# Performance work log

Measured on AMD Instinct MI355X. Metric: run time of the kernel, lower is better.

Reference implementation:

```python
import jax, jax.numpy as jnp
import numpy as np

B, D, C, H = 64, 64, 128, 64  # batch, feature dim, channels, MLP hidden

def setup_inputs() -> dict:
    key = jax.random.key(0)
    k1, k2, k3, kp = jax.random.split(key, 4)
    x = jax.random.normal(k1, (B, D, C), dtype=jnp.float32)
    W1 = jax.random.normal(k2, (2 * D, H), dtype=jnp.float32) / np.sqrt(2.0 * D).astype(np.float32)
    b1 = jnp.zeros((H,), jnp.float32)
    W2 = jax.random.normal(k3, (H, 1), dtype=jnp.float32) / np.sqrt(float(H)).astype(np.float32)
    b2 = jnp.zeros((1,), jnp.float32)
    perm = jax.random.permutation(kp, B)  # replaces torch.randperm(B)
    return {"x": x, "W1": W1, "b1": b1, "W2": W2, "b2": b2, "perm": perm}

def reference(x, W1, b1, W2, b2, perm):
    xt = jnp.transpose(x, (0, 2, 1))          # [B, C, D]
    b, c, d = xt.shape
    iu, ju = jnp.triu_indices(c, k=1)         # P = C*(C-1)//2 pairs (static)
    xi = xt[:, iu, :]                         # [B, P, D]
    xj = xt[:, ju, :]                         # [B, P, D]

    def T(h):                                  # h: [B, P, 2D] -> [B, P]
        z = jax.nn.relu(jnp.einsum('bpd,dh->bph', h, W1) + b1)
        return jnp.einsum('bph,ho->bp', z, W2) + b2[0]

    joint_term = T(jnp.concatenate([xi, xj], axis=-1))            # [B, P]
    marginal_term = T(jnp.concatenate([xi, xj[perm]], axis=-1))   # [B, P]
    lse = jax.nn.logsumexp(marginal_term, axis=0)                 # [P]
    mi_per_pair = joint_term - lse + jnp.log(jnp.float32(b))      # [B, P]
    total_mi = mi_per_pair.sum(axis=1).mean()
    n_pairs = c * (c - 1) // 2
    return -total_mi / n_pairs
```

## Files before the change

### kernel.cpp

```cpp
#include <hip/hip_runtime.h>
#include <hip/hip_bf16.h>
#include <math.h>

#define CC 128
#define BB 64
#define DD 64
#define HH 64
#define NPAIRS 8128
#define CHUNK 4
#define NBLK2 (NPAIRS / CHUNK)

struct Slots { double j; double l; };

#define OFF(i) ((i)*127 - ((i)*((i)-1))/2)

__global__ __launch_bounds__(256) void k1_tables(
    const float* __restrict__ x, const float* __restrict__ W1,
    const float* __restrict__ b1,
    float* __restrict__ A1, float* __restrict__ B2)
{
    __shared__ float xs[64][32];
    __shared__ float w1s[128][64];
    int b  = blockIdx.x >> 2;
    int cq = blockIdx.x & 3;

    for (int idx = threadIdx.x; idx < 2048; idx += 256)
        ((float4*)w1s)[idx] = ((const float4*)W1)[idx];
    for (int idx = threadIdx.x; idx < 2048; idx += 256) {
        int d = idx >> 5, cl = idx & 31;
        xs[d][cl] = x[((size_t)b * 64 + d) * 128 + cq * 32 + cl];
    }
    __syncthreads();

    int h  = threadIdx.x & 63;
    int c0 = (threadIdx.x >> 6) * 8;

    float accA[8] = {0,0,0,0,0,0,0,0};
    float accB[8] = {0,0,0,0,0,0,0,0};
    for (int d = 0; d < 64; ++d) {
        float wa = w1s[d][h];
        float wb = w1s[64 + d][h];
        float xv[8];
        *(float4*)&xv[0] = *(const float4*)&xs[d][c0];
        *(float4*)&xv[4] = *(const float4*)&xs[d][c0 + 4];
        #pragma unroll
        for (int k = 0; k < 8; ++k) {
            accA[k] = fmaf(xv[k], wa, accA[k]);
            accB[k] = fmaf(xv[k], wb, accB[k]);
        }
    }
    float bias = b1[h];
    #pragma unroll
    for (int k = 0; k < 8; ++k) {
        int c = cq * 32 + c0 + k;
        size_t o = ((size_t)b * CC + c) * HH + h;
        A1[o] = accA[k] + bias;
        B2[o] = accB[k];
    }
}

__global__ __launch_bounds__(64) void k2_pairs(
    const float* __restrict__ A1, const float* __restrict__ B2,
    const int* __restrict__ perm, const float* __restrict__ W2,
    Slots* __restrict__ slots)
{
    int lane = threadIdx.x;
    __shared__ int invp_s[64];
    invp_s[perm[lane]] = lane;
    __syncthreads();
    int ip = invp_s[lane];

    const float4* __restrict__ W2v = (const float4*)W2;

    float4 a1r[16], a2r[16];
    float accJ[CHUNK], accM[CHUNK];

    int p0 = blockIdx.x * CHUNK;
    double tt = 127.5 - sqrt(127.5 * 127.5 - 2.0 * (double)p0);
    int i = (int)tt;
    if (i < 0) i = 0;
    if (i > 126) i = 126;
    while (i < 126 && OFF(i + 1) <= p0) ++i;
    while (i > 0 && OFF(i) > p0) --i;
    int j = i + 1 + (p0 - OFF(i));

    bool need_load = true;
    for (int k = 0; k < CHUNK; ++k) {
        if (need_load) {
            const float4* ar1 = (const float4*)(A1 + ((size_t)lane * CC + i) * HH);
            const float4* ar2 = (const float4*)(A1 + ((size_t)ip   * CC + i) * HH);
            #pragma unroll
            for (int q = 0; q < 16; ++q) { a1r[q] = ar1[q]; a2r[q] = ar2[q]; }
            need_load = false;
        }
        const float4* br = (const float4*)(B2 + ((size_t)lane * CC + j) * HH);
        float aJ = 0.f, aM = 0.f;
        #pragma unroll
        for (int q = 0; q < 16; ++q) {
            float4 bq = br[q];
            float4 w  = W2v[q];
            aJ = fmaf(fmaxf(a1r[q].x + bq.x, 0.f), w.x, aJ);
            aJ = fmaf(fmaxf(a1r[q].y + bq.y, 0.f), w.y, aJ);
            aJ = fmaf(fmaxf(a1r[q].z + bq.z, 0.f), w.z, aJ);
            aJ = fmaf(fmaxf(a1r[q].w + bq.w, 0.f), w.w, aJ);
            aM = fmaf(fmaxf(a2r[q].x + bq.x, 0.f), w.x, aM);
            aM = fmaf(fmaxf(a2r[q].y + bq.y, 0.f), w.y, aM);
            aM = fmaf(fmaxf(a2r[q].z + bq.z, 0.f), w.z, aM);
            aM = fmaf(fmaxf(a2r[q].w + bq.w, 0.f), w.w, aM);
        }
        accJ[k] = aJ; accM[k] = aM;
        ++j;
        if (j == CC) { ++i; j = i + 1; need_load = true; }
    }

    float m[CHUNK], e[CHUNK];
    #pragma unroll
    for (int k = 0; k < CHUNK; ++k) m[k] = accM[k];
    #pragma unroll
    for (int off = 32; off > 0; off >>= 1) {
        #pragma unroll
        for (int k = 0; k < CHUNK; ++k)
            m[k] = fmaxf(m[k], __shfl_xor(m[k], off));
    }
    #pragma unroll
    for (int k = 0; k < CHUNK; ++k) e[k] = __expf(accM[k] - m[k]);
    #pragma unroll
    for (int off = 32; off > 0; off >>= 1) {
        #pragma unroll
        for (int k = 0; k < CHUNK; ++k)
            e[k] += __shfl_xor(e[k], off);
    }
    float lsum = 0.f;
    #pragma unroll
    for (int k = 0; k < CHUNK; ++k) lsum += m[k] + __logf(e[k]);

    float js = 0.f;
    #pragma unroll
    for (int k = 0; k < CHUNK; ++k) js += accJ[k];
    #pragma unroll
    for (int off = 32; off > 0; off >>= 1)
        js += __shfl_xor(js, off);

    if (lane == 0) { slots[blockIdx.x].j = (double)js; slots[blockIdx.x].l = (double)lsum; }
}

__global__ __launch_bounds__(256) void k3_final(
    const Slots* __restrict__ slots, float* __restrict__ out)
{
    __shared__ double sj[4], sl[4];
    double jd = 0.0, ld = 0.0;
    for (int s = threadIdx.x; s < NBLK2; s += 256) {
        jd += slots[s].j;
        ld += slots[s].l;
    }
    #pragma unroll
    for (int off = 32; off > 0; off >>= 1) {
        jd += __shfl_xor(jd, off);
        ld += __shfl_xor(ld, off);
    }
    int w = threadIdx.x >> 6;
    if ((threadIdx.x & 63) == 0) { sj[w] = jd; sl[w] = ld; }
    __syncthreads();
    if (threadIdx.x == 0) {
        jd = sj[0] + sj[1] + sj[2] + sj[3];
        ld = sl[0] + sl[1] + sl[2] + sl[3];
        double total = jd / 64.0 - ld + 8128.0 * log(64.0);
        out[0] = (float)(-total / 8128.0);
    }
}

extern "C" void kernel_launch(void* const* d_in, const int* in_sizes, int n_in,
                              void* d_out, int out_size, void* d_ws, size_t ws_size,
                              hipStream_t stream)
{
    const float* x   = (const float*)d_in[0];
    const float* W1  = (const float*)d_in[1];
    const float* b1  = (const float*)d_in[2];
    const float* W2  = (const float*)d_in[3];
    const int*  perm = (const int*)d_in[5];

    char* ws = (char*)d_ws;
    Slots* slots = (Slots*)ws;
    float* A1 = (float*)(ws + 40960);
    float* B2 = A1 + (size_t)BB * CC * HH;

    k1_tables<<<256, 256, 0, stream>>>(x, W1, b1, A1, B2);
    k2_pairs<<<NBLK2, 64, 0, stream>>>(A1, B2, perm, W2, slots);
    k3_final<<<1, 256, 0, stream>>>(slots, (float*)d_out);
}
```

Baseline: 104.6 us.

## Tile channel pairs into 4x4 blocks with LDS-staged B2 slabs

The pair kernel now gives each 256-thread block a 4x4 tile of upper-triangular channel pairs, 528 tiles in all, with one wave per row channel i. The B2 rows for the four j channels are staged once in swizzled shared memory and reused by all four waves. Each wave's A1 rows stay in registers across the four j values. Previously every pair reloaded its B2 row from global memory per lane, so this cuts global traffic by roughly the tile factor. The cost is some wasted arithmetic on the diagonal tiles, which is masked out, plus an extra block-level reduction and LDS use.

```diff
diff --git a/kernel.cpp b/kernel.cpp
--- a/kernel.cpp
+++ b/kernel.cpp
@@ -6,13 +6,10 @@
 #define BB 64
 #define DD 64
 #define HH 64
-#define NPAIRS 8128
-#define CHUNK 4
-#define NBLK2 (NPAIRS / CHUNK)
+#define NTILE 32
+#define NBLK2 528
 
 struct Slots { double j; double l; };
-
-#define OFF(i) ((i)*127 - ((i)*((i)-1))/2)
 
 __global__ __launch_bounds__(256) void k1_tables(
     const float* __restrict__ x, const float* __restrict__ W1,
@@ -59,89 +56,111 @@
     }
 }
 
-__global__ __launch_bounds__(64) void k2_pairs(
+__global__ __launch_bounds__(256, 2) void k2_pairs(
     const float* __restrict__ A1, const float* __restrict__ B2,
     const int* __restrict__ perm, const float* __restrict__ W2,
     Slots* __restrict__ slots)
 {
-    int lane = threadIdx.x;
+    __shared__ float4 bslab[4][64][16];
     __shared__ int invp_s[64];
+    __shared__ float wj[4], wl[4];
+
+    int t    = threadIdx.x;
+    int lane = t & 63;
+    int w    = t >> 6;
+
     invp_s[perm[lane]] = lane;
-    __syncthreads();
     int ip = invp_s[lane];
 
+    int u = blockIdx.x;
+    int r = 0;
+    while (((r + 1) * NTILE - ((r + 1) * r) / 2) <= u) ++r;
+    int tj = r + (u - (r * NTILE - (r * (r - 1)) / 2));
+    int i0 = r * 4, j0 = tj * 4;
+    bool diag = (tj == r);
+    int i = i0 + w;
+
+    const float4* a1p = (const float4*)(A1 + (size_t)lane * 8192 + (size_t)i * 64);
+    const float4* a2p = (const float4*)(A1 + (size_t)ip   * 8192 + (size_t)i * 64);
+    float4 a1r[16], a2r[16];
+    #pragma unroll
+    for (int q = 0; q < 16; ++q) a1r[q] = a1p[q];
+    #pragma unroll
+    for (int q = 0; q < 16; ++q) a2r[q] = a2p[q];
+
+    #pragma unroll
+    for (int rr = 0; rr < 16; ++rr) {
+        int fidx = rr * 256 + t;
+        int s = fidx >> 10;
+        int b = (fidx >> 4) & 63;
+        int q = fidx & 15;
+        float4 v = *(const float4*)(B2 + (size_t)b * 8192 + (size_t)(j0 + s) * 64 + (size_t)q * 4);
+        bslab[s][b][q ^ (b & 15)] = v;
+    }
+    __syncthreads();
+
     const float4* __restrict__ W2v = (const float4*)W2;
 
-    float4 a1r[16], a2r[16];
-    float accJ[CHUNK], accM[CHUNK];
-
-    int p0 = blockIdx.x * CHUNK;
-    double tt = 127.5 - sqrt(127.5 * 127.5 - 2.0 * (double)p0);
-    int i = (int)tt;
-    if (i < 0) i = 0;
-    if (i > 126) i = 126;
-    while (i < 126 && OFF(i + 1) <= p0) ++i;
-    while (i > 0 && OFF(i) > p0) --i;
-    int j = i + 1 + (p0 - OFF(i));
-
-    bool need_load = true;
-    for (int k = 0; k < CHUNK; ++k) {
-        if (need_load) {
-            const float4* ar1 = (const float4*)(A1 + ((size_t)lane * CC + i) * HH);
-            const float4* ar2 = (const float4*)(A1 + ((size_t)ip   * CC + i) * HH);
-            #pragma unroll
-            for (int q = 0; q < 16; ++q) { a1r[q] = ar1[q]; a2r[q] = ar2[q]; }
-            need_load = false;
+    float accJ[4], accM[4];
+    #pragma unroll
+    for (int jl = 0; jl < 4; ++jl) {
+        float aJ = 0.f, aM = 0.f;
+        #pragma unroll
+        for (int q = 0; q < 16; ++q) {
+            float4 bq = bslab[jl][lane][q ^ (lane & 15)];
+            float4 wv = W2v[q];
+            aJ = fmaf(fmaxf(a1r[q].x + bq.x, 0.f), wv.x, aJ);
+            aJ = fmaf(fmaxf(a1r[q].y + bq.y, 0.f), wv.y, aJ);
+            aJ = fmaf(fmaxf(a1r[q].z + bq.z, 0.f), wv.z, aJ);
+            aJ = fmaf(fmaxf(a1r[q].w + bq.w, 0.f), wv.w, aJ);
+            aM = fmaf(fmaxf(a2r[q].x + bq.x, 0.f), wv.x, aM);
+            aM = fmaf(fmaxf(a2r[q].y + bq.y, 0.f), wv.y, aM);
+            aM = fmaf(fmaxf(a2r[q].z + bq.z, 0.f), wv.z, aM);
+            aM = fmaf(fmaxf(a2r[q].w + bq.w, 0.f), wv.w, aM);
         }
-        const float4* br = (const float4*)(B2 + ((size_t)lane * CC + j) * HH);
-        float aJ = 0.f, aM = 0.f;
-        #pragma unroll
-        for (int q = 0; q < 16; ++q) {
-            float4 bq = br[q];
-            float4 w  = W2v[q];
-            aJ = fmaf(fmaxf(a1r[q].x + bq.x, 0.f), w.x, aJ);
-            aJ = fmaf(fmaxf(a1r[q].y + bq.y, 0.f), w.y, aJ);
-            aJ = fmaf(fmaxf(a1r[q].z + bq.z, 0.f), w.z, aJ);
-            aJ = fmaf(fmaxf(a1r[q].w + bq.w, 0.f), w.w, aJ);
-            aM = fmaf(fmaxf(a2r[q].x + bq.x, 0.f), w.x, aM);
-            aM = fmaf(fmaxf(a2r[q].y + bq.y, 0.f), w.y, aM);
-            aM = fmaf(fmaxf(a2r[q].z + bq.z, 0.f), w.z, aM);
-            aM = fmaf(fmaxf(a2r[q].w + bq.w, 0.f), w.w, aM);
+        accJ[jl] = aJ;
+        accM[jl] = aM;
+    }
+
+    float m[4], e[4];
+    #pragma unroll
+    for (int jl = 0; jl < 4; ++jl) m[jl] = accM[jl];
+    #pragma unroll
+    for (int off = 32; off > 0; off >>= 1) {
+        #pragma unroll
+        for (int jl = 0; jl < 4; ++jl)
+            m[jl] = fmaxf(m[jl], __shfl_xor(m[jl], off));
+    }
+    #pragma unroll
+    for (int jl = 0; jl < 4; ++jl) e[jl] = __expf(accM[jl] - m[jl]);
+    #pragma unroll
+    for (int off = 32; off > 0; off >>= 1) {
+        #pragma unroll
+        for (int jl = 0; jl < 4; ++jl)
+            e[jl] += __shfl_xor(e[jl], off);
+    }
+
+    float js = 0.f, lsum = 0.f;
+    #pragma unroll
+    for (int jl = 0; jl < 4; ++jl) {
+        bool valid = (!diag) || (jl > w);
+        if (valid) {
+            js   += accJ[jl];
+            lsum += m[jl] + __logf(e[jl]);
         }
-        accJ[k] = aJ; accM[k] = aM;
-        ++j;
-        if (j == CC) { ++i; j = i + 1; need_load = true; }
-    }
-
-    float m[CHUNK], e[CHUNK];
-    #pragma unroll
-    for (int k = 0; k < CHUNK; ++k) m[k] = accM[k];
-    #pragma unroll
-    for (int off = 32; off > 0; off >>= 1) {
-        #pragma unroll
-        for (int k = 0; k < CHUNK; ++k)
-            m[k] = fmaxf(m[k], __shfl_xor(m[k], off));
-    }
-    #pragma unroll
-    for (int k = 0; k < CHUNK; ++k) e[k] = __expf(accM[k] - m[k]);
-    #pragma unroll
-    for (int off = 32; off > 0; off >>= 1) {
-        #pragma unroll
-        for (int k = 0; k < CHUNK; ++k)
-            e[k] += __shfl_xor(e[k], off);
-    }
-    float lsum = 0.f;
-    #pragma unroll
-    for (int k = 0; k < CHUNK; ++k) lsum += m[k] + __logf(e[k]);
-
-    float js = 0.f;
-    #pragma unroll
-    for (int k = 0; k < CHUNK; ++k) js += accJ[k];
+    }
     #pragma unroll
     for (int off = 32; off > 0; off >>= 1)
         js += __shfl_xor(js, off);
 
-    if (lane == 0) { slots[blockIdx.x].j = (double)js; slots[blockIdx.x].l = (double)lsum; }
+    if (lane == 0) { wj[w] = js; wl[w] = lsum; }
+    __syncthreads();
+    if (t == 0) {
+        double jd = (double)wj[0] + (double)wj[1] + (double)wj[2] + (double)wj[3];
+        double ld = (double)wl[0] + (double)wl[1] + (double)wl[2] + (double)wl[3];
+        slots[blockIdx.x].j = jd;
+        slots[blockIdx.x].l = ld;
+    }
 }
 
 __global__ __launch_bounds__(256) void k3_final(
@@ -185,6 +204,6 @@
     float* B2 = A1 + (size_t)BB * CC * HH;
 
     k1_tables<<<256, 256, 0, stream>>>(x, W1, b1, A1, B2);
-    k2_pairs<<<NBLK2, 64, 0, stream>>>(A1, B2, perm, W2, slots);
+    k2_pairs<<<NBLK2, 256, 0, stream>>>(A1, B2, perm, W2, slots);
     k3_final<<<1, 256, 0, stream>>>(slots, (float*)d_out);
 }
```

After: 122.0 us. +16.7%, slower.
